# Kernel optimization log

Measured on AMD Instinct MI355X. Metric: run time of the kernel, lower is better.

The kernel has to match this reference:

```python
import jax, jax.numpy as jnp
import numpy as np

N_NODES = 50000
N_EDGES = 800000
D_IN = 256
D_HID = 256
D_OUT = 8


def _glorot(key, shape):
    fan_in = shape[-1]
    bound = 1.0 / np.sqrt(fan_in)
    return jax.random.uniform(key, shape, minval=-bound, maxval=bound, dtype=jnp.float32)


def setup_inputs() -> dict:
    key = jax.random.key(0)
    ks = jax.random.split(key, 12)
    x = jax.random.normal(ks[0], (N_NODES, D_IN), dtype=jnp.float32)
    edge_index = jax.random.randint(ks[1], (2, N_EDGES), 0, N_NODES, dtype=jnp.int64)
    return {
        "x": x,
        "edge_index": edge_index,
        # SAGEConv1: lin_l (neighbor path, has bias), lin_r (root path, no bias)
        "W1l": _glorot(ks[2], (D_HID, D_IN)),
        "b1": jnp.zeros((D_HID,), jnp.float32),
        "W1r": _glorot(ks[3], (D_HID, D_IN)),
        # SAGEConv2
        "W2l": _glorot(ks[4], (D_HID, D_HID)),
        "b2": jnp.zeros((D_HID,), jnp.float32),
        "W2r": _glorot(ks[5], (D_HID, D_HID)),
        # MLP decoder
        "Wm1": _glorot(ks[6], (D_HID, D_HID)),
        "bm1": _glorot(ks[7], (D_HID,)),
        "Wm2": _glorot(ks[8], (D_OUT, D_HID)),
        "bm2": _glorot(ks[9], (D_OUT,)),
    }


def _sage_conv(x, edge_index, Wl, b, Wr):
    # PyG SAGEConv with mean aggregation:
    # out = lin_l(mean_{j in N(i)} x_j) + lin_r(x_i)
    src, dst = edge_index[0], edge_index[1]
    msg = x[src]  # [E, d] gather
    agg = jax.ops.segment_sum(msg, dst, num_segments=x.shape[0])  # [N, d]
    cnt = jax.ops.segment_sum(jnp.ones((edge_index.shape[1],), x.dtype), dst,
                              num_segments=x.shape[0])  # in-degree [N]
    mean = agg / jnp.maximum(cnt, 1.0)[:, None]
    return mean @ Wl.T + b + x @ Wr.T


def reference(x, edge_index, W1l, b1, W1r, W2l, b2, W2r, Wm1, bm1, Wm2, bm2):
    h = jax.nn.relu(_sage_conv(x, edge_index, W1l, b1, W1r))
    h = jax.nn.relu(_sage_conv(h, edge_index, W2l, b2, W2r))
    h = jax.nn.relu(h @ Wm1.T + bm1)
    logits = h @ Wm2.T + bm2
    return jax.nn.softmax(logits, axis=-1)
```

## Files before the change

kernel.cpp:

```cpp
#include <hip/hip_runtime.h>
#include <hip/hip_bf16.h>
#include <cstdint>
#include <cstddef>

#define D 256

typedef __attribute__((ext_vector_type(8))) short bf16x8;
typedef __attribute__((ext_vector_type(4))) float f32x4;
typedef __attribute__((ext_vector_type(4))) unsigned short ushort4v;
typedef __attribute__((ext_vector_type(8))) unsigned short ushort8v;

__device__ __forceinline__ unsigned short f2bf(float f) {
  union { float f; unsigned int u; } v; v.f = f;
  unsigned int u = v.u;
  u += ((u >> 16) & 1u) + 0x7fffu;
  return (unsigned short)(u >> 16);
}
__device__ __forceinline__ float bf2f(unsigned short s) {
  union { unsigned int u; float f; } v; v.u = ((unsigned int)s) << 16;
  return v.f;
}

#define GLL16(g, l) __builtin_amdgcn_global_load_lds( \
    (const __attribute__((address_space(1))) void*)(g), \
    (__attribute__((address_space(3))) void*)(l), 16, 0, 0)


__global__ __launch_bounds__(256) void k_deg(const int* __restrict__ dst,
                                             int* __restrict__ deg, int E) {
  int e = blockIdx.x * 256 + threadIdx.x;
  if (e < E) atomicAdd(&deg[dst[e]], 1);
}

__global__ __launch_bounds__(256) void k_bsum(const int* __restrict__ deg,
                                              int* __restrict__ bsum, int M) {
  __shared__ int sm[256];
  int tid = threadIdx.x;
  int base = blockIdx.x * 1024 + tid * 4;
  int s = 0;
#pragma unroll
  for (int i = 0; i < 4; ++i) s += (base + i < M) ? deg[base + i] : 0;
  sm[tid] = s;
  __syncthreads();
  for (int off = 128; off > 0; off >>= 1) {
    if (tid < off) sm[tid] += sm[tid + off];
    __syncthreads();
  }
  if (tid == 0) bsum[blockIdx.x] = sm[0];
}

__global__ __launch_bounds__(64) void k_scanb(const int* __restrict__ bsum,
                                              int* __restrict__ boff,
                                              int* __restrict__ row_ptr,
                                              int nb, int M) {
  int l = threadIdx.x;
  int orig = (l < nb) ? bsum[l] : 0;
  int v = orig;
  for (int off = 1; off < 64; off <<= 1) {
    int t = __shfl_up(v, off);
    if (l >= off) v += t;
  }
  if (l < nb) boff[l] = v - orig;
  if (l == nb - 1) row_ptr[M] = v;
}

__global__ __launch_bounds__(256) void k_apply(const int* __restrict__ deg,
                                               const int* __restrict__ boff,
                                               int* __restrict__ row_ptr,
                                               int* __restrict__ cursor, int M) {
  __shared__ int sm[256];
  int tid = threadIdx.x;
  int base = blockIdx.x * 1024 + tid * 4;
  int d[4], p[4];
#pragma unroll
  for (int i = 0; i < 4; ++i) d[i] = (base + i < M) ? deg[base + i] : 0;
  p[0] = 0; p[1] = d[0]; p[2] = d[0] + d[1]; p[3] = d[0] + d[1] + d[2];
  int s = p[3] + d[3];
  sm[tid] = s;
  __syncthreads();
  for (int off = 1; off < 256; off <<= 1) {
    int t = (tid >= off) ? sm[tid - off] : 0;
    __syncthreads();
    sm[tid] += t;
    __syncthreads();
  }
  int excl = sm[tid] - s + boff[blockIdx.x];
#pragma unroll
  for (int i = 0; i < 4; ++i) {
    if (base + i < M) {
      row_ptr[base + i] = excl + p[i];
      cursor[base + i] = excl + p[i];
    }
  }
}

__global__ __launch_bounds__(256) void k_fill(const int* __restrict__ src,
                                              const int* __restrict__ dst,
                                              int* __restrict__ cursor,
                                              int* __restrict__ col, int E) {
  int e = blockIdx.x * 256 + threadIdx.x;
  if (e < E) {
    int p = atomicAdd(&cursor[dst[e]], 1);
    col[p] = src[e];
  }
}


__global__ __launch_bounds__(256) void k_split(const float* __restrict__ in,
                                               unsigned short* __restrict__ oh,
                                               unsigned short* __restrict__ ol,
                                               int n4) {
  int i = blockIdx.x * 256 + threadIdx.x;
  if (i >= n4) return;
  float4 v = ((const float4*)in)[i];
  float a[4] = {v.x, v.y, v.z, v.w};
  ushort4v h, l;
#pragma unroll
  for (int j = 0; j < 4; ++j) {
    h[j] = f2bf(a[j]);
    l[j] = f2bf(a[j] - bf2f(h[j]));
  }
  ((ushort4v*)oh)[i] = h;
  ((ushort4v*)ol)[i] = l;
}

__global__ __launch_bounds__(256) void k_splitw(
    const float* __restrict__ s0, const float* __restrict__ s1,
    const float* __restrict__ s2, const float* __restrict__ s3,
    const float* __restrict__ s4,
    unsigned short* __restrict__ h0, unsigned short* __restrict__ l0,
    unsigned short* __restrict__ h1, unsigned short* __restrict__ l1,
    unsigned short* __restrict__ h2, unsigned short* __restrict__ l2,
    unsigned short* __restrict__ h3, unsigned short* __restrict__ l3,
    unsigned short* __restrict__ h4, unsigned short* __restrict__ l4) {
  const float* s; unsigned short* oh; unsigned short* ol;
  switch (blockIdx.y) {
    case 0: s = s0; oh = h0; ol = l0; break;
    case 1: s = s1; oh = h1; ol = l1; break;
    case 2: s = s2; oh = h2; ol = l2; break;
    case 3: s = s3; oh = h3; ol = l3; break;
    default: s = s4; oh = h4; ol = l4; break;
  }
  int i = blockIdx.x * 256 + threadIdx.x;
  float4 v = ((const float4*)s)[i];
  float a[4] = {v.x, v.y, v.z, v.w};
  ushort4v h, l;
#pragma unroll
  for (int j = 0; j < 4; ++j) {
    h[j] = f2bf(a[j]);
    l[j] = f2bf(a[j] - bf2f(h[j]));
  }
  ((ushort4v*)oh)[i] = h;
  ((ushort4v*)ol)[i] = l;
}


__global__ __launch_bounds__(256) void k_gemm_mfma(
    const unsigned short* __restrict__ Ah, const unsigned short* __restrict__ Al,
    const unsigned short* __restrict__ Wh, const unsigned short* __restrict__ Wl,
    unsigned short* __restrict__ outBF, float* __restrict__ outF32,
    const float* __restrict__ bias, int M, int NBF, int NF, int relu,
    int nbxshift) {
  __shared__ char lds[65536];

  const int tid = threadIdx.x;
  const int wave = tid >> 6;
  const int lane = tid & 63;

  int nwg = gridDim.x;
  int id = blockIdx.x;
  int q = nwg >> 3, r = nwg & 7;
  int xcd = id & 7, j = id >> 3;
  int w = ((xcd < r) ? xcd * (q + 1) : r * (q + 1) + (xcd - r) * q) + j;
  const int by = w >> nbxshift;
  const int bx = w & ((1 << nbxshift) - 1);
  const int n0 = bx * 128;

  int aoff[2], woff[2], ldso[2];
#pragma unroll
  for (int rr = 0; rr < 2; ++rr) {
    int o = rr * 4096 + wave * 1024 + lane * 16;
    int row = o >> 6;
    int sp = (o >> 4) & 3;
    int sl = sp ^ ((row >> 1) & 3);
    int arow = by * 128 + row; if (arow > M - 1) arow = M - 1;
    aoff[rr] = arow * 256 + sl * 8;
    woff[rr] = (n0 + row) * 256 + sl * 8;
    ldso[rr] = rr * 4096 + wave * 1024;
  }

  const int rbase = (wave >> 1) * 64;
  const int cbase = (wave & 1) * 64;
  const int fr = lane & 15;
  const int g = lane >> 4;

  int a_addr[4], w_addr[4];
#pragma unroll
  for (int m = 0; m < 4; ++m) {
    int row = rbase + m * 16 + fr;
    a_addr[m] = row * 64 + ((g ^ ((row >> 1) & 3)) * 16);
  }
#pragma unroll
  for (int n = 0; n < 4; ++n) {
    int row = cbase + n * 16 + fr;
    w_addr[n] = row * 64 + ((g ^ ((row >> 1) & 3)) * 16);
  }

  f32x4 acc[4][4] = {};

#pragma unroll
  for (int rr = 0; rr < 2; ++rr) {
    GLL16(Ah + aoff[rr], lds + 0     + ldso[rr]);
    GLL16(Al + aoff[rr], lds + 8192  + ldso[rr]);
    GLL16(Wh + woff[rr], lds + 16384 + ldso[rr]);
    GLL16(Wl + woff[rr], lds + 24576 + ldso[rr]);
  }

  for (int t = 0; t < 8; ++t) {
    const int cb = (t & 1) * 32768;
    if (t < 7) {
      const int nb = ((t + 1) & 1) * 32768;
      const int ko = (t + 1) * 32;
#pragma unroll
      for (int rr = 0; rr < 2; ++rr) {
        GLL16(Ah + aoff[rr] + ko, lds + nb + 0     + ldso[rr]);
        GLL16(Al + aoff[rr] + ko, lds + nb + 8192  + ldso[rr]);
        GLL16(Wh + woff[rr] + ko, lds + nb + 16384 + ldso[rr]);
        GLL16(Wl + woff[rr] + ko, lds + nb + 24576 + ldso[rr]);
      }
      asm volatile("s_waitcnt vmcnt(8)" ::: "memory");
    } else {
      asm volatile("s_waitcnt vmcnt(0)" ::: "memory");
    }
    __builtin_amdgcn_s_barrier();

    bf16x8 ah[4], al[4], wh[4], wl[4];
#pragma unroll
    for (int m = 0; m < 4; ++m) {
      ah[m] = *(const bf16x8*)(lds + cb + 0    + a_addr[m]);
      al[m] = *(const bf16x8*)(lds + cb + 8192 + a_addr[m]);
    }
#pragma unroll
    for (int n = 0; n < 4; ++n) {
      wh[n] = *(const bf16x8*)(lds + cb + 16384 + w_addr[n]);
      wl[n] = *(const bf16x8*)(lds + cb + 24576 + w_addr[n]);
    }
#pragma unroll
    for (int m = 0; m < 4; ++m)
#pragma unroll
      for (int n = 0; n < 4; ++n) {
        acc[m][n] = __builtin_amdgcn_mfma_f32_16x16x32_bf16(ah[m], wh[n], acc[m][n], 0, 0, 0);
        acc[m][n] = __builtin_amdgcn_mfma_f32_16x16x32_bf16(ah[m], wl[n], acc[m][n], 0, 0, 0);
        acc[m][n] = __builtin_amdgcn_mfma_f32_16x16x32_bf16(al[m], wh[n], acc[m][n], 0, 0, 0);
      }
    __builtin_amdgcn_s_barrier();
  }

#pragma unroll
  for (int n = 0; n < 4; ++n) {
    int col = n0 + cbase + n * 16 + fr;
    bool isbf = col < NBF;
    int fcol = col - NBF;
    float bv = (!isbf && bias) ? bias[fcol] : 0.f;
#pragma unroll
    for (int m = 0; m < 4; ++m) {
      f32x4 a = acc[m][n];
#pragma unroll
      for (int rr = 0; rr < 4; ++rr) {
        int row = by * 128 + rbase + m * 16 + g * 4 + rr;
        if (row < M) {
          if (isbf) {
            outBF[(size_t)row * NBF + col] = f2bf(a[rr]);
          } else {
            float v = a[rr] + bv;
            if (relu) v = fmaxf(v, 0.f);
            outF32[(size_t)row * NF + fcol] = v;
          }
        }
      }
    }
  }
}


__global__ __launch_bounds__(256) void k_agg2(const unsigned short* __restrict__ T1,
                                              const float* __restrict__ T2,
                                              unsigned short* __restrict__ Hh,
                                              unsigned short* __restrict__ Hl,
                                              const int* __restrict__ row_ptr,
                                              const int* __restrict__ col, int M) {
  int wave = threadIdx.x >> 6, lane = threadIdx.x & 63;
  int n = blockIdx.x * 4 + wave;
  if (n >= M) return;
  int beg = row_ptr[n], end = row_ptr[n + 1];
  int half = lane >> 5, sl = lane & 31;
  float s[8] = {0.f, 0.f, 0.f, 0.f, 0.f, 0.f, 0.f, 0.f};
  int j = beg + half;
  for (; j + 2 < end; j += 4) {
    int i0 = col[j];
    int i1 = col[j + 2];
    ushort8v v0 = *(const ushort8v*)(T1 + (size_t)i0 * 256 + sl * 8);
    ushort8v v1 = *(const ushort8v*)(T1 + (size_t)i1 * 256 + sl * 8);
#pragma unroll
    for (int i = 0; i < 8; ++i) s[i] += bf2f(v0[i]) + bf2f(v1[i]);
  }
  for (; j < end; j += 2) {
    int i0 = col[j];
    ushort8v v0 = *(const ushort8v*)(T1 + (size_t)i0 * 256 + sl * 8);
#pragma unroll
    for (int i = 0; i < 8; ++i) s[i] += bf2f(v0[i]);
  }
#pragma unroll
  for (int i = 0; i < 8; ++i) s[i] += __shfl_xor(s[i], 32);
  int dg = end - beg;
  float inv = 1.0f / (float)(dg > 0 ? dg : 1);
  const float4* t2p = (const float4*)(T2 + (size_t)n * 256 + sl * 8);
  float4 ta = t2p[0], tb = t2p[1];
  float h[8];
  h[0] = fmaxf(s[0] * inv + ta.x, 0.f);
  h[1] = fmaxf(s[1] * inv + ta.y, 0.f);
  h[2] = fmaxf(s[2] * inv + ta.z, 0.f);
  h[3] = fmaxf(s[3] * inv + ta.w, 0.f);
  h[4] = fmaxf(s[4] * inv + tb.x, 0.f);
  h[5] = fmaxf(s[5] * inv + tb.y, 0.f);
  h[6] = fmaxf(s[6] * inv + tb.z, 0.f);
  h[7] = fmaxf(s[7] * inv + tb.w, 0.f);
  if (half == 0) {
    ushort8v hh;
#pragma unroll
    for (int i = 0; i < 8; ++i) hh[i] = f2bf(h[i]);
    *(ushort8v*)(Hh + (size_t)n * 256 + sl * 8) = hh;
  } else {
    ushort8v hl;
#pragma unroll
    for (int i = 0; i < 8; ++i) {
      unsigned short hi = f2bf(h[i]);
      hl[i] = f2bf(h[i] - bf2f(hi));
    }
    *(ushort8v*)(Hl + (size_t)n * 256 + sl * 8) = hl;
  }
}


__global__ __launch_bounds__(256) void k_final(const float* __restrict__ H,
                                               const float* __restrict__ Wm2,
                                               const float* __restrict__ bm2,
                                               float* __restrict__ out, int M) {
  int node = blockIdx.x * 4 + (threadIdx.x >> 6);
  int lane = threadIdx.x & 63;
  if (node >= M) return;
  int o = lane >> 3;
  int r = lane & 7;
  const float* h = H + (size_t)node * D;
  const float* w = Wm2 + (size_t)o * D;
  float p = 0.f;
  for (int k = r; k < D; k += 8) p += h[k] * w[k];
  p += __shfl_xor(p, 1);
  p += __shfl_xor(p, 2);
  p += __shfl_xor(p, 4);
  float logit = p + bm2[o];
  float m = logit;
  m = fmaxf(m, __shfl_xor(m, 8));
  m = fmaxf(m, __shfl_xor(m, 16));
  m = fmaxf(m, __shfl_xor(m, 32));
  float e = expf(logit - m);
  float s = e;
  s += __shfl_xor(s, 8);
  s += __shfl_xor(s, 16);
  s += __shfl_xor(s, 32);
  if (r == 0) out[(size_t)node * 8 + o] = e / s;
}


extern "C" void kernel_launch(void* const* d_in, const int* in_sizes, int n_in,
                              void* d_out, int out_size, void* d_ws, size_t ws_size,
                              hipStream_t stream) {
  const float* x   = (const float*)d_in[0];
  const int*   ei  = (const int*)d_in[1];
  const float* W1l = (const float*)d_in[2];
  const float* b1  = (const float*)d_in[3];
  const float* W1r = (const float*)d_in[4];
  const float* W2l = (const float*)d_in[5];
  const float* b2  = (const float*)d_in[6];
  const float* W2r = (const float*)d_in[7];
  const float* Wm1 = (const float*)d_in[8];
  const float* bm1 = (const float*)d_in[9];
  const float* Wm2 = (const float*)d_in[10];
  const float* bm2 = (const float*)d_in[11];
  float* out = (float*)d_out;

  int M = in_sizes[0] / D;
  int E = in_sizes[1] / 2;
  const int* src = ei;
  const int* dst = ei + E;

  char* p = (char*)d_ws;
  auto alloc = [&](size_t bytes) {
    char* q = p;
    p += (bytes + 255) & ~(size_t)255;
    return q;
  };
  unsigned short* bh0  = (unsigned short*)alloc((size_t)M * 256 * 2);
  unsigned short* bh1  = (unsigned short*)alloc((size_t)M * 256 * 2);
  unsigned short* T1bf = (unsigned short*)alloc((size_t)M * 256 * 2);
  float*          T2f  = (float*)alloc((size_t)M * 256 * 4);
  unsigned short* Wc1h = (unsigned short*)alloc(512 * 256 * 2);
  unsigned short* Wc1l = (unsigned short*)alloc(512 * 256 * 2);
  unsigned short* Wc2h = (unsigned short*)alloc(512 * 256 * 2);
  unsigned short* Wc2l = (unsigned short*)alloc(512 * 256 * 2);
  unsigned short* Wm1h = (unsigned short*)alloc(256 * 256 * 2);
  unsigned short* Wm1l = (unsigned short*)alloc(256 * 256 * 2);
  int* deg     = (int*)alloc((size_t)M * 4);
  int* row_ptr = (int*)alloc((size_t)(M + 1) * 4);
  int* cursor  = (int*)alloc((size_t)M * 4);
  int* col     = (int*)alloc((size_t)E * 4);
  int* bsum    = (int*)alloc(64 * 4);
  int* boff    = (int*)alloc(64 * 4);

  int nb = (M + 1023) / 1024;

  hipMemsetAsync(deg, 0, (size_t)M * sizeof(int), stream);
  k_deg<<<dim3((E + 255) / 256), dim3(256), 0, stream>>>(dst, deg, E);
  k_bsum<<<dim3(nb), dim3(256), 0, stream>>>(deg, bsum, M);
  k_scanb<<<dim3(1), dim3(64), 0, stream>>>(bsum, boff, row_ptr, nb, M);
  k_apply<<<dim3(nb), dim3(256), 0, stream>>>(deg, boff, row_ptr, cursor, M);
  k_fill<<<dim3((E + 255) / 256), dim3(256), 0, stream>>>(src, dst, cursor, col, E);

  int nx4 = M * 256 / 4;
  k_split<<<dim3((nx4 + 255) / 256), dim3(256), 0, stream>>>(x, bh0, bh1, nx4);
  k_splitw<<<dim3(64, 5), dim3(256), 0, stream>>>(
      W1l, W1r, W2l, W2r, Wm1,
      Wc1h, Wc1l, Wc1h + 65536, Wc1l + 65536,
      Wc2h, Wc2l, Wc2h + 65536, Wc2l + 65536,
      Wm1h, Wm1l);

  dim3 blk(256);
  int nwg4 = ((M + 127) / 128) * 4;
  int nwg2 = ((M + 127) / 128) * 2;
  int aggGrid = (M + 3) / 4;

  k_gemm_mfma<<<dim3(nwg4), blk, 0, stream>>>(bh0, bh1, Wc1h, Wc1l, T1bf, T2f, b1, M, 256, 256, 0, 2);
  k_agg2<<<dim3(aggGrid), blk, 0, stream>>>(T1bf, T2f, bh0, bh1, row_ptr, col, M);
  k_gemm_mfma<<<dim3(nwg4), blk, 0, stream>>>(bh0, bh1, Wc2h, Wc2l, T1bf, T2f, b2, M, 256, 256, 0, 2);
  k_agg2<<<dim3(aggGrid), blk, 0, stream>>>(T1bf, T2f, bh0, bh1, row_ptr, col, M);
  k_gemm_mfma<<<dim3(nwg2), blk, 0, stream>>>(bh0, bh1, Wm1h, Wm1l, nullptr, T2f, bm1, M, 0, 256, 1, 1);
  k_final<<<dim3((M + 3) / 4), blk, 0, stream>>>(T2f, Wm2, bm2, out, M);
}
```

Before: 571.0 us.

## Fuse CSR build into cooperative kernel, merge splits, emit bf16 MLP hidden

The separate memset, degree, scan and fill kernels become one cooperative kernel that uses grid-wide syncs, which removes several launches. The x and weight split kernels are merged into one launch. The MLP hidden GEMM now writes a bf16 output with bias and ReLU fused, and the final kernel reads it with vector loads. This cuts the traffic of an fp32 intermediate, at the cost of grid.sync overhead, fewer CSR threads (1024 blocks) and bf16 rounding of the hidden layer.

```diff
diff --git a/kernel.cpp b/kernel.cpp
--- a/kernel.cpp
+++ b/kernel.cpp
@@ -1,7 +1,10 @@
 #include <hip/hip_runtime.h>
 #include <hip/hip_bf16.h>
+#include <hip/hip_cooperative_groups.h>
 #include <cstdint>
 #include <cstddef>
+
+namespace cg = cooperative_groups;
 
 #define D 256
 
@@ -26,122 +29,116 @@
     (__attribute__((address_space(3))) void*)(l), 16, 0, 0)
 
 
-__global__ __launch_bounds__(256) void k_deg(const int* __restrict__ dst,
-                                             int* __restrict__ deg, int E) {
-  int e = blockIdx.x * 256 + threadIdx.x;
-  if (e < E) atomicAdd(&deg[dst[e]], 1);
-}
-
-__global__ __launch_bounds__(256) void k_bsum(const int* __restrict__ deg,
-                                              int* __restrict__ bsum, int M) {
+__global__ __launch_bounds__(256) void k_csr(const int* __restrict__ src,
+                                             const int* __restrict__ dst,
+                                             int* __restrict__ deg,
+                                             int* __restrict__ row_ptr,
+                                             int* __restrict__ cursor,
+                                             int* __restrict__ col,
+                                             int* __restrict__ bsum,
+                                             int* __restrict__ boff,
+                                             int M, int E, int nb) {
+  cg::grid_group grid = cg::this_grid();
   __shared__ int sm[256];
-  int tid = threadIdx.x;
-  int base = blockIdx.x * 1024 + tid * 4;
-  int s = 0;
-#pragma unroll
-  for (int i = 0; i < 4; ++i) s += (base + i < M) ? deg[base + i] : 0;
-  sm[tid] = s;
-  __syncthreads();
-  for (int off = 128; off > 0; off >>= 1) {
-    if (tid < off) sm[tid] += sm[tid + off];
+  const int tid = threadIdx.x;
+  const int bid = blockIdx.x;
+  const int gsz = gridDim.x * 256;
+  const int gtid = bid * 256 + tid;
+
+  for (int i = gtid; i < M; i += gsz) deg[i] = 0;
+  grid.sync();
+
+  for (int e = gtid; e < E; e += gsz) atomicAdd(&deg[dst[e]], 1);
+  grid.sync();
+
+  if (bid < nb) {
+    int base = bid * 1024 + tid * 4;
+    int s = 0;
+#pragma unroll
+    for (int i = 0; i < 4; ++i) s += (base + i < M) ? deg[base + i] : 0;
+    sm[tid] = s;
     __syncthreads();
-  }
-  if (tid == 0) bsum[blockIdx.x] = sm[0];
-}
-
-__global__ __launch_bounds__(64) void k_scanb(const int* __restrict__ bsum,
-                                              int* __restrict__ boff,
-                                              int* __restrict__ row_ptr,
-                                              int nb, int M) {
-  int l = threadIdx.x;
-  int orig = (l < nb) ? bsum[l] : 0;
-  int v = orig;
-  for (int off = 1; off < 64; off <<= 1) {
-    int t = __shfl_up(v, off);
-    if (l >= off) v += t;
-  }
-  if (l < nb) boff[l] = v - orig;
-  if (l == nb - 1) row_ptr[M] = v;
-}
-
-__global__ __launch_bounds__(256) void k_apply(const int* __restrict__ deg,
-                                               const int* __restrict__ boff,
-                                               int* __restrict__ row_ptr,
-                                               int* __restrict__ cursor, int M) {
-  __shared__ int sm[256];
-  int tid = threadIdx.x;
-  int base = blockIdx.x * 1024 + tid * 4;
-  int d[4], p[4];
-#pragma unroll
-  for (int i = 0; i < 4; ++i) d[i] = (base + i < M) ? deg[base + i] : 0;
-  p[0] = 0; p[1] = d[0]; p[2] = d[0] + d[1]; p[3] = d[0] + d[1] + d[2];
-  int s = p[3] + d[3];
-  sm[tid] = s;
-  __syncthreads();
-  for (int off = 1; off < 256; off <<= 1) {
-    int t = (tid >= off) ? sm[tid - off] : 0;
+    for (int off = 128; off > 0; off >>= 1) {
+      if (tid < off) sm[tid] += sm[tid + off];
+      __syncthreads();
+    }
+    if (tid == 0) bsum[bid] = sm[0];
+  }
+  grid.sync();
+
+  if (bid == 0 && tid < 64) {
+    int l = tid;
+    int orig = (l < nb) ? bsum[l] : 0;
+    int v = orig;
+    for (int off = 1; off < 64; off <<= 1) {
+      int t = __shfl_up(v, off);
+      if (l >= off) v += t;
+    }
+    if (l < nb) boff[l] = v - orig;
+    if (l == nb - 1) row_ptr[M] = v;
+  }
+  grid.sync();
+
+  if (bid < nb) {
+    int base = bid * 1024 + tid * 4;
+    int d[4], p[4];
+#pragma unroll
+    for (int i = 0; i < 4; ++i) d[i] = (base + i < M) ? deg[base + i] : 0;
+    p[0] = 0; p[1] = d[0]; p[2] = d[0] + d[1]; p[3] = d[0] + d[1] + d[2];
+    int s = p[3] + d[3];
+    sm[tid] = s;
     __syncthreads();
-    sm[tid] += t;
-    __syncthreads();
-  }
-  int excl = sm[tid] - s + boff[blockIdx.x];
-#pragma unroll
-  for (int i = 0; i < 4; ++i) {
-    if (base + i < M) {
-      row_ptr[base + i] = excl + p[i];
-      cursor[base + i] = excl + p[i];
-    }
-  }
-}
-
-__global__ __launch_bounds__(256) void k_fill(const int* __restrict__ src,
-                                              const int* __restrict__ dst,
-                                              int* __restrict__ cursor,
-                                              int* __restrict__ col, int E) {
-  int e = blockIdx.x * 256 + threadIdx.x;
-  if (e < E) {
+    for (int off = 1; off < 256; off <<= 1) {
+      int t = (tid >= off) ? sm[tid - off] : 0;
+      __syncthreads();
+      sm[tid] += t;
+      __syncthreads();
+    }
+    int excl = sm[tid] - s + boff[bid];
+#pragma unroll
+    for (int i = 0; i < 4; ++i) {
+      if (base + i < M) {
+        row_ptr[base + i] = excl + p[i];
+        cursor[base + i] = excl + p[i];
+      }
+    }
+  }
+  grid.sync();
+
+  for (int e = gtid; e < E; e += gsz) {
     int p = atomicAdd(&cursor[dst[e]], 1);
     col[p] = src[e];
   }
 }
 
 
-__global__ __launch_bounds__(256) void k_split(const float* __restrict__ in,
-                                               unsigned short* __restrict__ oh,
-                                               unsigned short* __restrict__ ol,
-                                               int n4) {
-  int i = blockIdx.x * 256 + threadIdx.x;
-  if (i >= n4) return;
-  float4 v = ((const float4*)in)[i];
-  float a[4] = {v.x, v.y, v.z, v.w};
-  ushort4v h, l;
-#pragma unroll
-  for (int j = 0; j < 4; ++j) {
-    h[j] = f2bf(a[j]);
-    l[j] = f2bf(a[j] - bf2f(h[j]));
-  }
-  ((ushort4v*)oh)[i] = h;
-  ((ushort4v*)ol)[i] = l;
-}
-
-__global__ __launch_bounds__(256) void k_splitw(
-    const float* __restrict__ s0, const float* __restrict__ s1,
-    const float* __restrict__ s2, const float* __restrict__ s3,
-    const float* __restrict__ s4,
-    unsigned short* __restrict__ h0, unsigned short* __restrict__ l0,
-    unsigned short* __restrict__ h1, unsigned short* __restrict__ l1,
-    unsigned short* __restrict__ h2, unsigned short* __restrict__ l2,
-    unsigned short* __restrict__ h3, unsigned short* __restrict__ l3,
-    unsigned short* __restrict__ h4, unsigned short* __restrict__ l4) {
-  const float* s; unsigned short* oh; unsigned short* ol;
-  switch (blockIdx.y) {
-    case 0: s = s0; oh = h0; ol = l0; break;
-    case 1: s = s1; oh = h1; ol = l1; break;
-    case 2: s = s2; oh = h2; ol = l2; break;
-    case 3: s = s3; oh = h3; ol = l3; break;
-    default: s = s4; oh = h4; ol = l4; break;
-  }
-  int i = blockIdx.x * 256 + threadIdx.x;
+__global__ __launch_bounds__(256) void k_splitall(
+    const float* __restrict__ x, int nx4, int nxb,
+    const float* __restrict__ W1l, const float* __restrict__ W1r,
+    const float* __restrict__ W2l, const float* __restrict__ W2r,
+    const float* __restrict__ Wm1,
+    unsigned short* __restrict__ xh, unsigned short* __restrict__ xl,
+    unsigned short* __restrict__ c1h, unsigned short* __restrict__ c1l,
+    unsigned short* __restrict__ c2h, unsigned short* __restrict__ c2l,
+    unsigned short* __restrict__ m1h, unsigned short* __restrict__ m1l) {
+  const float* s; unsigned short* oh; unsigned short* ol; int i, lim;
+  int bid = blockIdx.x;
+  if (bid < nxb) {
+    s = x; oh = xh; ol = xl;
+    i = bid * 256 + threadIdx.x; lim = nx4;
+  } else {
+    int wb = bid - nxb;
+    int w = wb >> 6;
+    i = (wb & 63) * 256 + threadIdx.x; lim = 16384;
+    switch (w) {
+      case 0: s = W1l; oh = c1h;         ol = c1l;         break;
+      case 1: s = W1r; oh = c1h + 65536; ol = c1l + 65536; break;
+      case 2: s = W2l; oh = c2h;         ol = c2l;         break;
+      case 3: s = W2r; oh = c2h + 65536; ol = c2l + 65536; break;
+      default: s = Wm1; oh = m1h;        ol = m1l;         break;
+    }
+  }
+  if (i >= lim) return;
   float4 v = ((const float4*)s)[i];
   float a[4] = {v.x, v.y, v.z, v.w};
   ushort4v h, l;
@@ -159,8 +156,8 @@
     const unsigned short* __restrict__ Ah, const unsigned short* __restrict__ Al,
     const unsigned short* __restrict__ Wh, const unsigned short* __restrict__ Wl,
     unsigned short* __restrict__ outBF, float* __restrict__ outF32,
-    const float* __restrict__ bias, int M, int NBF, int NF, int relu,
-    int nbxshift) {
+    const float* __restrict__ biasF, const float* __restrict__ biasB,
+    int M, int NBF, int NF, int relu, int nbxshift) {
   __shared__ char lds[65536];
 
   const int tid = threadIdx.x;
@@ -219,14 +216,14 @@
   for (int t = 0; t < 8; ++t) {
     const int cb = (t & 1) * 32768;
     if (t < 7) {
-      const int nb = ((t + 1) & 1) * 32768;
+      const int nbuf = ((t + 1) & 1) * 32768;
       const int ko = (t + 1) * 32;
 #pragma unroll
       for (int rr = 0; rr < 2; ++rr) {
-        GLL16(Ah + aoff[rr] + ko, lds + nb + 0     + ldso[rr]);
-        GLL16(Al + aoff[rr] + ko, lds + nb + 8192  + ldso[rr]);
-        GLL16(Wh + woff[rr] + ko, lds + nb + 16384 + ldso[rr]);
-        GLL16(Wl + woff[rr] + ko, lds + nb + 24576 + ldso[rr]);
+        GLL16(Ah + aoff[rr] + ko, lds + nbuf + 0     + ldso[rr]);
+        GLL16(Al + aoff[rr] + ko, lds + nbuf + 8192  + ldso[rr]);
+        GLL16(Wh + woff[rr] + ko, lds + nbuf + 16384 + ldso[rr]);
+        GLL16(Wl + woff[rr] + ko, lds + nbuf + 24576 + ldso[rr]);
       }
       asm volatile("s_waitcnt vmcnt(8)" ::: "memory");
     } else {
@@ -256,22 +253,38 @@
     __builtin_amdgcn_s_barrier();
   }
 
-#pragma unroll
-  for (int n = 0; n < 4; ++n) {
-    int col = n0 + cbase + n * 16 + fr;
-    bool isbf = col < NBF;
-    int fcol = col - NBF;
-    float bv = (!isbf && bias) ? bias[fcol] : 0.f;
-#pragma unroll
-    for (int m = 0; m < 4; ++m) {
-      f32x4 a = acc[m][n];
-#pragma unroll
-      for (int rr = 0; rr < 4; ++rr) {
-        int row = by * 128 + rbase + m * 16 + g * 4 + rr;
-        if (row < M) {
-          if (isbf) {
-            outBF[(size_t)row * NBF + col] = f2bf(a[rr]);
-          } else {
+  if (n0 < NBF) {
+#pragma unroll
+    for (int n = 0; n < 4; ++n) {
+      int col = n0 + cbase + n * 16 + fr;
+      float bvb = biasB ? biasB[col] : 0.f;
+#pragma unroll
+      for (int m = 0; m < 4; ++m) {
+        f32x4 a = acc[m][n];
+#pragma unroll
+        for (int rr = 0; rr < 4; ++rr) {
+          int row = by * 128 + rbase + m * 16 + g * 4 + rr;
+          if (row < M) {
+            float v = a[rr] + bvb;
+            if (biasB) v = fmaxf(v, 0.f);
+            outBF[(size_t)row * NBF + col] = f2bf(v);
+          }
+        }
+      }
+    }
+  } else {
+#pragma unroll
+    for (int n = 0; n < 4; ++n) {
+      int col = n0 + cbase + n * 16 + fr;
+      int fcol = col - NBF;
+      float bv = biasF ? biasF[fcol] : 0.f;
+#pragma unroll
+      for (int m = 0; m < 4; ++m) {
+        f32x4 a = acc[m][n];
+#pragma unroll
+        for (int rr = 0; rr < 4; ++rr) {
+          int row = by * 128 + rbase + m * 16 + g * 4 + rr;
+          if (row < M) {
             float v = a[rr] + bv;
             if (relu) v = fmaxf(v, 0.f);
             outF32[(size_t)row * NF + fcol] = v;
@@ -342,7 +355,7 @@
 }
 
 
-__global__ __launch_bounds__(256) void k_final(const float* __restrict__ H,
+__global__ __launch_bounds__(256) void k_final(const unsigned short* __restrict__ H,
                                                const float* __restrict__ Wm2,
                                                const float* __restrict__ bm2,
                                                float* __restrict__ out, int M) {
@@ -351,10 +364,17 @@
   if (node >= M) return;
   int o = lane >> 3;
   int r = lane & 7;
-  const float* h = H + (size_t)node * D;
-  const float* w = Wm2 + (size_t)o * D;
+  const unsigned short* h = H + (size_t)node * D + r * 32;
+  const float* w = Wm2 + (size_t)o * D + r * 32;
   float p = 0.f;
-  for (int k = r; k < D; k += 8) p += h[k] * w[k];
+#pragma unroll
+  for (int c = 0; c < 4; ++c) {
+    ushort8v hv = ((const ushort8v*)h)[c];
+    float4 w0 = ((const float4*)w)[c * 2];
+    float4 w1 = ((const float4*)w)[c * 2 + 1];
+    p += bf2f(hv[0]) * w0.x + bf2f(hv[1]) * w0.y + bf2f(hv[2]) * w0.z + bf2f(hv[3]) * w0.w;
+    p += bf2f(hv[4]) * w1.x + bf2f(hv[5]) * w1.y + bf2f(hv[6]) * w1.z + bf2f(hv[7]) * w1.w;
+  }
   p += __shfl_xor(p, 1);
   p += __shfl_xor(p, 2);
   p += __shfl_xor(p, 4);
@@ -364,11 +384,11 @@
   m = fmaxf(m, __shfl_xor(m, 16));
   m = fmaxf(m, __shfl_xor(m, 32));
   float e = expf(logit - m);
-  float s = e;
-  s += __shfl_xor(s, 8);
-  s += __shfl_xor(s, 16);
-  s += __shfl_xor(s, 32);
-  if (r == 0) out[(size_t)node * 8 + o] = e / s;
+  float ssum = e;
+  ssum += __shfl_xor(ssum, 8);
+  ssum += __shfl_xor(ssum, 16);
+  ssum += __shfl_xor(ssum, 32);
+  if (r == 0) out[(size_t)node * 8 + o] = e / ssum;
 }
 
 
@@ -419,30 +439,33 @@
 
   int nb = (M + 1023) / 1024;
 
-  hipMemsetAsync(deg, 0, (size_t)M * sizeof(int), stream);
-  k_deg<<<dim3((E + 255) / 256), dim3(256), 0, stream>>>(dst, deg, E);
-  k_bsum<<<dim3(nb), dim3(256), 0, stream>>>(deg, bsum, M);
-  k_scanb<<<dim3(1), dim3(64), 0, stream>>>(bsum, boff, row_ptr, nb, M);
-  k_apply<<<dim3(nb), dim3(256), 0, stream>>>(deg, boff, row_ptr, cursor, M);
-  k_fill<<<dim3((E + 255) / 256), dim3(256), 0, stream>>>(src, dst, cursor, col, E);
+  {
+    const int* srcv = src; const int* dstv = dst;
+    int Mv = M, Ev = E, nbv = nb;
+    void* args[] = {(void*)&srcv, (void*)&dstv, (void*)&deg, (void*)&row_ptr,
+                    (void*)&cursor, (void*)&col, (void*)&bsum, (void*)&boff,
+                    (void*)&Mv, (void*)&Ev, (void*)&nbv};
+    hipLaunchCooperativeKernel((void*)k_csr, dim3(1024), dim3(256), args, 0, stream);
+  }
 
   int nx4 = M * 256 / 4;
-  k_split<<<dim3((nx4 + 255) / 256), dim3(256), 0, stream>>>(x, bh0, bh1, nx4);
-  k_splitw<<<dim3(64, 5), dim3(256), 0, stream>>>(
-      W1l, W1r, W2l, W2r, Wm1,
-      Wc1h, Wc1l, Wc1h + 65536, Wc1l + 65536,
-      Wc2h, Wc2l, Wc2h + 65536, Wc2l + 65536,
-      Wm1h, Wm1l);
+  int nxb = (nx4 + 255) / 256;
+  k_splitall<<<dim3(nxb + 5 * 64), dim3(256), 0, stream>>>(
+      x, nx4, nxb, W1l, W1r, W2l, W2r, Wm1,
+      bh0, bh1, Wc1h, Wc1l, Wc2h, Wc2l, Wm1h, Wm1l);
 
   dim3 blk(256);
   int nwg4 = ((M + 127) / 128) * 4;
   int nwg2 = ((M + 127) / 128) * 2;
   int aggGrid = (M + 3) / 4;
 
-  k_gemm_mfma<<<dim3(nwg4), blk, 0, stream>>>(bh0, bh1, Wc1h, Wc1l, T1bf, T2f, b1, M, 256, 256, 0, 2);
+  k_gemm_mfma<<<dim3(nwg4), blk, 0, stream>>>(bh0, bh1, Wc1h, Wc1l, T1bf, T2f,
+                                              b1, nullptr, M, 256, 256, 0, 2);
   k_agg2<<<dim3(aggGrid), blk, 0, stream>>>(T1bf, T2f, bh0, bh1, row_ptr, col, M);
-  k_gemm_mfma<<<dim3(nwg4), blk, 0, stream>>>(bh0, bh1, Wc2h, Wc2l, T1bf, T2f, b2, M, 256, 256, 0, 2);
+  k_gemm_mfma<<<dim3(nwg4), blk, 0, stream>>>(bh0, bh1, Wc2h, Wc2l, T1bf, T2f,
+                                              b2, nullptr, M, 256, 256, 0, 2);
   k_agg2<<<dim3(aggGrid), blk, 0, stream>>>(T1bf, T2f, bh0, bh1, row_ptr, col, M);
-  k_gemm_mfma<<<dim3(nwg2), blk, 0, stream>>>(bh0, bh1, Wm1h, Wm1l, nullptr, T2f, bm1, M, 0, 256, 1, 1);
-  k_final<<<dim3((M + 3) / 4), blk, 0, stream>>>(T2f, Wm2, bm2, out, M);
-}
+  k_gemm_mfma<<<dim3(nwg2), blk, 0, stream>>>(bh0, bh1, Wm1h, Wm1l, T1bf, nullptr,
+                                              nullptr, bm1, M, 256, 0, 1, 1);
+  k_final<<<dim3((M + 3) / 4), blk, 0, stream>>>(T1bf, Wm2, bm2, out, M);
+}
```

After: 1.061 ms. 85.7% more time.
